# Kernel optimization log

Measured on AMD Instinct MI355X. Metric: run time of the kernel, lower is better.

Reference implementation:

```python
import jax, jax.numpy as jnp
import numpy as np

L = 4096
D = 150  # TRANSITION_STATE_OUTPUTS_DIM


def setup_inputs() -> dict:
    key = jax.random.key(0)
    k1, k2 = jax.random.split(key)
    adj = jax.random.uniform(k1, (L, L, 2), dtype=jnp.float32)
    h = jax.random.normal(k2, (L, D), dtype=jnp.float32)
    return {"unpreprocessed_unweight_adj_matrix": adj, "h": h}


def reference(unpreprocessed_unweight_adj_matrix, h):
    # Original math: h_in[j,d]  = sum_{i,e} adj[i,j,e] * h[i,d]
    #                h_out[i,d] = sum_{j,e} adj[i,j,e] * h[j,d]
    # Contract the 2 edge types first, then a single [L,L]x[L,D] matmul each way,
    # avoiding the O(L^2 * 2 * D) broadcasted intermediate of the original.
    n, d = h.shape
    A = unpreprocessed_unweight_adj_matrix.reshape(n, n, 2).sum(axis=2)  # [L, L]
    h_in = A.T @ h   # sum over source nodes i -> [L, D]
    h_out = A @ h    # sum over target nodes j -> [L, D]
    return (h_in, h_out)
```

## Files before the change

### kernel.cpp

```cpp
#include <hip/hip_runtime.h>

#define LN 4096
#define DN 150
#define NT 10
#define KSPLIT 4
#define KQ 1024
#define NSS 4

typedef __attribute__((ext_vector_type(8))) short bf16x8;
typedef __attribute__((ext_vector_type(4))) float f32x4;

__device__ __forceinline__ unsigned short f2bf(float f) {
    unsigned int u = __builtin_bit_cast(unsigned int, f);
    u = (u + 0x7FFFu + ((u >> 16) & 1u)) >> 16;
    return (unsigned short)u;
}

__global__ __launch_bounds__(256) void k_zero(f32x4* __restrict__ p, int n4) {
    int i = blockIdx.x * 256 + threadIdx.x;
    if (i < n4) p[i] = (f32x4){0.f, 0.f, 0.f, 0.f};
}

__global__ __launch_bounds__(256) void k_transpose(const float* __restrict__ h,
                                                   unsigned short* __restrict__ Ht) {
    __shared__ float S[64][33];
    const int i0 = blockIdx.x * 64;
    const int d0 = blockIdx.y * 32;
    const int tid = threadIdx.x;
    for (int t = tid; t < 64 * 32; t += 256) {
        int ii = t >> 5, dd = t & 31;
        int d = d0 + dd;
        S[ii][dd] = (d < DN) ? h[(size_t)(i0 + ii) * DN + d] : 0.0f;
    }
    __syncthreads();
    for (int t = tid; t < 32 * 64; t += 256) {
        int dd = t >> 6, ii = t & 63;
        Ht[(size_t)(d0 + dd) * LN + i0 + ii] = f2bf(S[ii][dd]);
    }
}

template <int TR>
__global__ __launch_bounds__(256, 2) void k_gemm(const float* __restrict__ adj,
                                                 const unsigned short* __restrict__ Ht,
                                                 float* __restrict__ out) {
    __shared__ unsigned short At[2][32 * 256];
    __shared__ float red[32][160];
    const int tid  = threadIdx.x;
    const int lane = tid & 63;
    const int wave = tid >> 6;
    const int r16  = lane & 15;
    const int g    = lane >> 4;
    const int m0 = blockIdx.x * 32;
    const int kq = blockIdx.y * KQ;

    f32x4 acc[2][NT];
    #pragma unroll
    for (int mt = 0; mt < 2; ++mt)
        #pragma unroll
        for (int n = 0; n < NT; ++n) acc[mt][n] = (f32x4){0.f, 0.f, 0.f, 0.f};

    f32x4 sv[16];

    auto stage_load = [&](int ss) {
        if (TR == 0) {
            const int row = tid >> 7;
            const int kk  = tid & 127;
            #pragma unroll
            for (int rr = 0; rr < 16; ++rr) {
                int rowr = rr * 2 + row;
                sv[rr] = *reinterpret_cast<const f32x4*>(
                    adj + ((size_t)(m0 + rowr) * LN + kq + ss * 256 + 2 * kk) * 2);
            }
        } else {
            const int iof = tid >> 4;
            const int jp  = tid & 15;
            #pragma unroll
            for (int rr = 0; rr < 16; ++rr) {
                int il = rr * 16 + iof;
                sv[rr] = *reinterpret_cast<const f32x4*>(
                    adj + ((size_t)(kq + ss * 256 + il) * LN + m0 + jp * 2) * 2);
            }
        }
    };
    auto stage_write = [&](int buf) {
        if (TR == 0) {
            const int row = tid >> 7;
            const int kk  = tid & 127;
            #pragma unroll
            for (int rr = 0; rr < 16; ++rr) {
                int rowr = rr * 2 + row;
                unsigned int u = (unsigned int)f2bf(sv[rr].x + sv[rr].y) |
                                 ((unsigned int)f2bf(sv[rr].z + sv[rr].w) << 16);
                *reinterpret_cast<unsigned int*>(
                    &At[buf][rowr * 256 + ((2 * kk) ^ ((rowr & 15) << 3))]) = u;
            }
        } else {
            const int iof = tid >> 4;
            const int jA  = (tid & 15) * 2, jB = jA + 1;
            #pragma unroll
            for (int rr = 0; rr < 16; ++rr) {
                int k = rr * 16 + iof;
                At[buf][jA * 256 + (k ^ ((jA & 15) << 3))] = f2bf(sv[rr].x + sv[rr].y);
                At[buf][jB * 256 + (k ^ ((jB & 15) << 3))] = f2bf(sv[rr].z + sv[rr].w);
            }
        }
    };
    auto frag = [&](int buf, int mt, int s) {
        int row  = mt * 16 + r16;
        int kloc = wave * 64 + s * 32 + g * 8;
        return *reinterpret_cast<const bf16x8*>(&At[buf][row * 256 + (kloc ^ (r16 << 3))]);
    };
    auto loadB = [&](bf16x8 (&bb)[NT], int ss, int s) {
        int k = kq + ss * 256 + wave * 64 + s * 32 + g * 8;
        #pragma unroll
        for (int n = 0; n < NT; ++n)
            bb[n] = *reinterpret_cast<const bf16x8*>(Ht + (size_t)(n * 16 + r16) * LN + k);
    };

    stage_load(0);
    stage_write(0);
    __syncthreads();
    for (int ss = 0; ss < NSS; ++ss) {
        const int buf = ss & 1;
        if (ss + 1 < NSS) stage_load(ss + 1);
        #pragma unroll
        for (int s = 0; s < 2; ++s) {
            bf16x8 B[NT];
            loadB(B, ss, s);
            bf16x8 a0 = frag(buf, 0, s);
            bf16x8 a1 = frag(buf, 1, s);
            #pragma unroll
            for (int n = 0; n < NT; ++n) {
                acc[0][n] = __builtin_amdgcn_mfma_f32_16x16x32_bf16(a0, B[n], acc[0][n], 0, 0, 0);
                acc[1][n] = __builtin_amdgcn_mfma_f32_16x16x32_bf16(a1, B[n], acc[1][n], 0, 0, 0);
            }
        }
        __syncthreads();
        if (ss + 1 < NSS) stage_write(buf ^ 1);
        __syncthreads();
    }

    for (int w4 = 0; w4 < 4; ++w4) {
        if (wave == w4) {
            #pragma unroll
            for (int mt = 0; mt < 2; ++mt)
                #pragma unroll
                for (int n = 0; n < NT; ++n)
                    #pragma unroll
                    for (int q = 0; q < 4; ++q) {
                        int row = mt * 16 + g * 4 + q;
                        if (w4 == 0) red[row][n * 16 + r16]  = acc[mt][n][q];
                        else         red[row][n * 16 + r16] += acc[mt][n][q];
                    }
        }
        __syncthreads();
    }
    for (int t2 = tid; t2 < 32 * DN; t2 += 256) {
        int row = t2 / DN, col = t2 % DN;
        atomicAdd(&out[(size_t)(m0 + row) * DN + col], red[row][col]);
    }
}

extern "C" void kernel_launch(void* const* d_in, const int* in_sizes, int n_in,
                              void* d_out, int out_size, void* d_ws, size_t ws_size,
                              hipStream_t stream) {
    const float* adj = (const float*)d_in[0];
    const float* h   = (const float*)d_in[1];
    float* out = (float*)d_out;
    unsigned short* Ht = (unsigned short*)d_ws;

    const int n4 = out_size / 4;
    k_zero<<<(n4 + 255) / 256, 256, 0, stream>>>((f32x4*)out, n4);
    k_transpose<<<dim3(64, 5), 256, 0, stream>>>(h, Ht);
    k_gemm<0><<<dim3(128, KSPLIT), 256, 0, stream>>>(adj, Ht, out + (size_t)LN * DN);
    k_gemm<1><<<dim3(128, KSPLIT), 256, 0, stream>>>(adj, Ht, out);
}
```

Measured before the change: 104.7 us.

## Retile GEMM so each wave owns distinct rows and drop LDS k-reduction

Each block now covers 64 output rows, with each wave owning 16 rows across the full K stage, in place of 32 rows with the K dimension split across waves. This removes the shared-memory cross-wave reduction and its barriers; each wave atomically adds its own accumulators directly. K-split doubles to 8 with smaller 128-wide stages, and the LDS layout is repacked as 32-bit words with a new swizzle. The trade-off is that each wave now loads the full B fragments for every k step, so global B traffic rises, and each wave has fewer independent MFMA chains.

```diff
diff --git a/kernel.cpp b/kernel.cpp
--- a/kernel.cpp
+++ b/kernel.cpp
@@ -3,17 +3,18 @@
 #define LN 4096
 #define DN 150
 #define NT 10
-#define KSPLIT 4
-#define KQ 1024
-#define NSS 4
+#define KSPLIT 8
+#define KQ (LN / KSPLIT)
+#define KS 128
+#define NSS (KQ / KS)
 
 typedef __attribute__((ext_vector_type(8))) short bf16x8;
 typedef __attribute__((ext_vector_type(4))) float f32x4;
 
-__device__ __forceinline__ unsigned short f2bf(float f) {
+__device__ __forceinline__ unsigned int f2bf(float f) {
     unsigned int u = __builtin_bit_cast(unsigned int, f);
     u = (u + 0x7FFFu + ((u >> 16) & 1u)) >> 16;
-    return (unsigned short)u;
+    return u & 0xFFFFu;
 }
 
 __global__ __launch_bounds__(256) void k_zero(f32x4* __restrict__ p, int n4) {
@@ -35,7 +36,7 @@
     __syncthreads();
     for (int t = tid; t < 32 * 64; t += 256) {
         int dd = t >> 6, ii = t & 63;
-        Ht[(size_t)(d0 + dd) * LN + i0 + ii] = f2bf(S[ii][dd]);
+        Ht[(size_t)(d0 + dd) * LN + i0 + ii] = (unsigned short)f2bf(S[ii][dd]);
     }
 }
 
@@ -43,121 +44,102 @@
 __global__ __launch_bounds__(256, 2) void k_gemm(const float* __restrict__ adj,
                                                  const unsigned short* __restrict__ Ht,
                                                  float* __restrict__ out) {
-    __shared__ unsigned short At[2][32 * 256];
-    __shared__ float red[32][160];
+    __shared__ unsigned int At[2][64 * 64];
     const int tid  = threadIdx.x;
     const int lane = tid & 63;
     const int wave = tid >> 6;
     const int r16  = lane & 15;
     const int g    = lane >> 4;
-    const int m0 = blockIdx.x * 32;
+    const int m0 = blockIdx.x * 64;
     const int kq = blockIdx.y * KQ;
 
-    f32x4 acc[2][NT];
+    f32x4 acc[NT];
     #pragma unroll
-    for (int mt = 0; mt < 2; ++mt)
-        #pragma unroll
-        for (int n = 0; n < NT; ++n) acc[mt][n] = (f32x4){0.f, 0.f, 0.f, 0.f};
+    for (int n = 0; n < NT; ++n) acc[n] = (f32x4){0.f, 0.f, 0.f, 0.f};
 
     f32x4 sv[16];
 
     auto stage_load = [&](int ss) {
+        const int kb = kq + ss * KS;
         if (TR == 0) {
-            const int row = tid >> 7;
-            const int kk  = tid & 127;
             #pragma unroll
             for (int rr = 0; rr < 16; ++rr) {
-                int rowr = rr * 2 + row;
+                int rl = rr * 4 + (tid >> 6);
                 sv[rr] = *reinterpret_cast<const f32x4*>(
-                    adj + ((size_t)(m0 + rowr) * LN + kq + ss * 256 + 2 * kk) * 2);
+                    adj + ((size_t)(m0 + rl) * LN + kb) * 2 + (tid & 63) * 4);
             }
         } else {
-            const int iof = tid >> 4;
-            const int jp  = tid & 15;
             #pragma unroll
-            for (int rr = 0; rr < 16; ++rr) {
-                int il = rr * 16 + iof;
-                sv[rr] = *reinterpret_cast<const f32x4*>(
-                    adj + ((size_t)(kq + ss * 256 + il) * LN + m0 + jp * 2) * 2);
+            for (int rr = 0; rr < 8; ++rr) {
+                int ip = rr * 8 + (tid >> 5);
+                size_t base = ((size_t)(kb + 2 * ip) * LN + m0 + 2 * (tid & 31)) * 2;
+                sv[2 * rr]     = *reinterpret_cast<const f32x4*>(adj + base);
+                sv[2 * rr + 1] = *reinterpret_cast<const f32x4*>(adj + base + 2 * LN);
             }
         }
     };
     auto stage_write = [&](int buf) {
         if (TR == 0) {
-            const int row = tid >> 7;
-            const int kk  = tid & 127;
+            const int kk = tid & 63;
             #pragma unroll
             for (int rr = 0; rr < 16; ++rr) {
-                int rowr = rr * 2 + row;
-                unsigned int u = (unsigned int)f2bf(sv[rr].x + sv[rr].y) |
-                                 ((unsigned int)f2bf(sv[rr].z + sv[rr].w) << 16);
-                *reinterpret_cast<unsigned int*>(
-                    &At[buf][rowr * 256 + ((2 * kk) ^ ((rowr & 15) << 3))]) = u;
+                int rl = rr * 4 + (tid >> 6);
+                unsigned int u = f2bf(sv[rr].x + sv[rr].y) | (f2bf(sv[rr].z + sv[rr].w) << 16);
+                At[buf][rl * 64 + (((kk >> 2) ^ ((rl >> 1) & 15)) & 15) * 4 + (kk & 3)] = u;
             }
         } else {
-            const int iof = tid >> 4;
-            const int jA  = (tid & 15) * 2, jB = jA + 1;
+            const int jA = 2 * (tid & 31), jB = jA + 1;
             #pragma unroll
-            for (int rr = 0; rr < 16; ++rr) {
-                int k = rr * 16 + iof;
-                At[buf][jA * 256 + (k ^ ((jA & 15) << 3))] = f2bf(sv[rr].x + sv[rr].y);
-                At[buf][jB * 256 + (k ^ ((jB & 15) << 3))] = f2bf(sv[rr].z + sv[rr].w);
+            for (int rr = 0; rr < 8; ++rr) {
+                int ip = rr * 8 + (tid >> 5);
+                f32x4 v0 = sv[2 * rr], v1 = sv[2 * rr + 1];
+                unsigned int uA = f2bf(v0.x + v0.y) | (f2bf(v1.x + v1.y) << 16);
+                unsigned int uB = f2bf(v0.z + v0.w) | (f2bf(v1.z + v1.w) << 16);
+                int bs = ((ip >> 2) ^ ((jA >> 1) & 15)) & 15;
+                At[buf][jA * 64 + bs * 4 + (ip & 3)] = uA;
+                At[buf][jB * 64 + bs * 4 + (ip & 3)] = uB;
             }
         }
     };
-    auto frag = [&](int buf, int mt, int s) {
-        int row  = mt * 16 + r16;
-        int kloc = wave * 64 + s * 32 + g * 8;
-        return *reinterpret_cast<const bf16x8*>(&At[buf][row * 256 + (kloc ^ (r16 << 3))]);
-    };
-    auto loadB = [&](bf16x8 (&bb)[NT], int ss, int s) {
-        int k = kq + ss * 256 + wave * 64 + s * 32 + g * 8;
-        #pragma unroll
-        for (int n = 0; n < NT; ++n)
-            bb[n] = *reinterpret_cast<const bf16x8*>(Ht + (size_t)(n * 16 + r16) * LN + k);
+    auto frag = [&](int buf, int s) {
+        int row = wave * 16 + r16;
+        int blk = s * 4 + g;
+        return *reinterpret_cast<const bf16x8*>(
+            &At[buf][row * 64 + ((blk ^ ((row >> 1) & 15)) & 15) * 4]);
     };
 
     stage_load(0);
     stage_write(0);
     __syncthreads();
+    #pragma unroll 2
     for (int ss = 0; ss < NSS; ++ss) {
         const int buf = ss & 1;
         if (ss + 1 < NSS) stage_load(ss + 1);
         #pragma unroll
-        for (int s = 0; s < 2; ++s) {
+        for (int s = 0; s < 4; ++s) {
+            const int k = kq + ss * KS + s * 32 + g * 8;
             bf16x8 B[NT];
-            loadB(B, ss, s);
-            bf16x8 a0 = frag(buf, 0, s);
-            bf16x8 a1 = frag(buf, 1, s);
             #pragma unroll
-            for (int n = 0; n < NT; ++n) {
-                acc[0][n] = __builtin_amdgcn_mfma_f32_16x16x32_bf16(a0, B[n], acc[0][n], 0, 0, 0);
-                acc[1][n] = __builtin_amdgcn_mfma_f32_16x16x32_bf16(a1, B[n], acc[1][n], 0, 0, 0);
-            }
+            for (int n = 0; n < NT; ++n)
+                B[n] = *reinterpret_cast<const bf16x8*>(Ht + (size_t)(n * 16 + r16) * LN + k);
+            bf16x8 a = frag(buf, s);
+            #pragma unroll
+            for (int n = 0; n < NT; ++n)
+                acc[n] = __builtin_amdgcn_mfma_f32_16x16x32_bf16(a, B[n], acc[n], 0, 0, 0);
         }
         __syncthreads();
         if (ss + 1 < NSS) stage_write(buf ^ 1);
         __syncthreads();
     }
 
-    for (int w4 = 0; w4 < 4; ++w4) {
-        if (wave == w4) {
-            #pragma unroll
-            for (int mt = 0; mt < 2; ++mt)
-                #pragma unroll
-                for (int n = 0; n < NT; ++n)
-                    #pragma unroll
-                    for (int q = 0; q < 4; ++q) {
-                        int row = mt * 16 + g * 4 + q;
-                        if (w4 == 0) red[row][n * 16 + r16]  = acc[mt][n][q];
-                        else         red[row][n * 16 + r16] += acc[mt][n][q];
-                    }
+    #pragma unroll
+    for (int n = 0; n < NT; ++n) {
+        #pragma unroll
+        for (int q = 0; q < 4; ++q) {
+            int row = m0 + wave * 16 + g * 4 + q;
+            int col = n * 16 + r16;
+            if (col < DN) atomicAdd(&out[(size_t)row * DN + col], acc[n][q]);
         }
-        __syncthreads();
-    }
-    for (int t2 = tid; t2 < 32 * DN; t2 += 256) {
-        int row = t2 / DN, col = t2 % DN;
-        atomicAdd(&out[(size_t)(m0 + row) * DN + col], red[row][col]);
     }
 }
 
@@ -172,6 +154,6 @@
     const int n4 = out_size / 4;
     k_zero<<<(n4 + 255) / 256, 256, 0, stream>>>((f32x4*)out, n4);
     k_transpose<<<dim3(64, 5), 256, 0, stream>>>(h, Ht);
-    k_gemm<0><<<dim3(128, KSPLIT), 256, 0, stream>>>(adj, Ht, out + (size_t)LN * DN);
-    k_gemm<1><<<dim3(128, KSPLIT), 256, 0, stream>>>(adj, Ht, out);
+    k_gemm<0><<<dim3(64, KSPLIT), 256, 0, stream>>>(adj, Ht, out + (size_t)LN * DN);
+    k_gemm<1><<<dim3(64, KSPLIT), 256, 0, stream>>>(adj, Ht, out);
 }
```

Result: slower. 158.3 us (+51.3%).
